# Optimization experiments

Hardware: AMD Instinct MI355X
Metric: run time of the kernel (lower is better)

The kernel has to match this reference:

```python
import jax, jax.numpy as jnp
import numpy as np


def setup_inputs() -> dict:
    key = jax.random.key(0)
    k1, k2 = jax.random.split(key)
    x = jax.random.normal(k1, (128, 128, 256), dtype=jnp.float32)
    embed = jax.random.normal(k2, (16384, 256), dtype=jnp.float32)
    return {"x": x, "embed": embed}


BETA = 0.25


def reference(x, embed):
    dim = embed.shape[1]
    n_embed = embed.shape[0]
    latent = x.reshape(-1, dim)  # [N, d]
    # squared euclidean distance: ||z||^2 - 2 z.e^T + ||e||^2  -> [N, K]
    dist = (
        jnp.sum(latent * latent, axis=1, keepdims=True)
        - 2.0 * jnp.einsum("nd,kd->nk", latent, embed)
        + jnp.sum(embed * embed, axis=1)[None, :]
    )
    embed_ind = jnp.argmax(-dist, axis=1)  # [N]
    # one-hot histogram of code usage (segment_sum == onehot.sum(0))
    embed_onehot_sum = jax.ops.segment_sum(
        jnp.ones_like(embed_ind, dtype=jnp.int32), embed_ind, num_segments=n_embed
    )
    unused_codes = jnp.sum(embed_onehot_sum == 0)
    x_q = embed[embed_ind].reshape(x.shape)
    quant_loss = jnp.mean((x_q - jax.lax.stop_gradient(x)) ** 2) + BETA * jnp.mean(
        (x - jax.lax.stop_gradient(x_q)) ** 2
    )
    # straight-through estimator
    x_q = x + jax.lax.stop_gradient(x_q - x)
    embed_ind = embed_ind.reshape(x.shape[:-1])
    return (x_q, quant_loss, unused_codes, embed_ind)
```

## Files before the change

kernel.cpp:

```cpp
#include <hip/hip_runtime.h>

#define N_LAT 16384
#define N_EMB 16384
#define DIM   256
#define XQ_ELEMS (N_LAT * DIM)

typedef __attribute__((ext_vector_type(8))) _Float16 f16x8;
typedef __attribute__((ext_vector_type(4))) float    f32x4;

#define SWZ(a) ((a) ^ ((((a) >> 6) & 7) << 4))

#define GLD16(g, l) __builtin_amdgcn_global_load_lds( \
    (const __attribute__((address_space(1))) unsigned int*)(g), \
    (__attribute__((address_space(3))) unsigned int*)(l), 16, 0, 0)


__global__ __launch_bounds__(256) void k_convert(const float* __restrict__ src,
                                                 char* __restrict__ hi,
                                                 char* __restrict__ lo,
                                                 float* __restrict__ norm) {
    const int gid = blockIdx.x * 256 + threadIdx.x;
    const int row = gid >> 5, k8 = gid & 31;
    const float* s = src + (size_t)row * DIM + k8 * 8;
    float f[8];
    *reinterpret_cast<float4*>(&f[0]) = *reinterpret_cast<const float4*>(s);
    *reinterpret_cast<float4*>(&f[4]) = *reinterpret_cast<const float4*>(s + 4);
    f16x8 hv, lv;
    double nrm = 0.0;
#pragma unroll
    for (int m = 0; m < 8; ++m) {
        const _Float16 h = (_Float16)f[m];
        hv[m] = h;
        lv[m] = (_Float16)(f[m] - (float)h);
        nrm += (double)f[m] * (double)f[m];
    }
    const int dst = ((row >> 7) * 8 + (k8 >> 2)) * 8192 + SWZ((row & 127) * 64 + (k8 & 3) * 16);
    *reinterpret_cast<f16x8*>(hi + dst) = hv;
    *reinterpret_cast<f16x8*>(lo + dst) = lv;
    if (norm) {
#pragma unroll
        for (int m = 16; m; m >>= 1) nrm += __shfl_xor(nrm, m, 64);
        if (k8 == 0) norm[row] = (float)nrm;
    }
}

__global__ __launch_bounds__(256) void k_argmin(const char* __restrict__ xhi,
                                                const char* __restrict__ xlo,
                                                const char* __restrict__ ehi,
                                                const char* __restrict__ elo,
                                                const float* __restrict__ enorm,
                                                unsigned long long* __restrict__ best) {
    __shared__ char smem[65536];
    char* const sm = smem;

    const int tid = threadIdx.x;
    const int w   = tid >> 6;
    const int l   = tid & 63;
    const int lg  = l >> 4;
    const int lr  = l & 15;

    const int row0 = blockIdx.x * 128;
    const int kc   = blockIdx.y;

    const size_t lane16 = (size_t)(w * 2048 + l * 16);
    const size_t gA  = (size_t)blockIdx.x * 65536 + lane16;
    const size_t gB0 = (size_t)kc * 8 * 65536 + lane16;

    auto STAGE = [&](int ct_, int ks_, int half) {
        const int    o  = half * 32768 + w * 2048;
        const size_t ga = gA + (size_t)ks_ * 8192;
        const size_t gb = gB0 + (size_t)ct_ * 65536 + (size_t)ks_ * 8192;
#pragma unroll
        for (int q = 0; q < 2; ++q) {
            GLD16(xhi + ga + q * 1024, sm + o +         q * 1024);
            GLD16(xlo + ga + q * 1024, sm + o +  8192 + q * 1024);
            GLD16(ehi + gb + q * 1024, sm + o + 16384 + q * 1024);
            GLD16(elo + gb + q * 1024, sm + o + 24576 + q * 1024);
        }
    };

    int aoff[2];
#pragma unroll
    for (int i = 0; i < 2; ++i)
        aoff[i] = SWZ((w * 32 + i * 16 + lr) * 64 + lg * 16);
    int boff[8];
#pragma unroll
    for (int j = 0; j < 8; ++j)
        boff[j] = SWZ((j * 16 + lr) * 64 + lg * 16);

    unsigned long long pmin[2][4];
#pragma unroll
    for (int i = 0; i < 2; ++i)
#pragma unroll
        for (int t = 0; t < 4; ++t) pmin[i][t] = ~0ULL;

    STAGE(0, 0, 0);
    __syncthreads();
    int half = 0;

    for (int ct = 0; ct < 8; ++ct) {
        f32x4 acc[2][8];
#pragma unroll
        for (int i = 0; i < 2; ++i)
#pragma unroll
            for (int j = 0; j < 8; ++j) acc[i][j] = (f32x4)0.0f;

        for (int ks = 0; ks < 8; ++ks) {
            int nks = ks + 1, nct = ct;
            if (nks == 8) { nks = 0; ++nct; }
            if (nct < 8) STAGE(nct, nks, half ^ 1);

            const int hb = half * 32768;
            f16x8 ah[2], al[2];
#pragma unroll
            for (int i = 0; i < 2; ++i) {
                ah[i] = *reinterpret_cast<const f16x8*>(sm + hb +        aoff[i]);
                al[i] = *reinterpret_cast<const f16x8*>(sm + hb + 8192 + aoff[i]);
            }
#pragma unroll
            for (int j = 0; j < 8; ++j) {
                const f16x8 bh = *reinterpret_cast<const f16x8*>(sm + hb + 16384 + boff[j]);
                const f16x8 bl = *reinterpret_cast<const f16x8*>(sm + hb + 24576 + boff[j]);
#pragma unroll
                for (int i = 0; i < 2; ++i) {
                    acc[i][j] = __builtin_amdgcn_mfma_f32_16x16x32_f16(ah[i], bh, acc[i][j], 0, 0, 0);
                    acc[i][j] = __builtin_amdgcn_mfma_f32_16x16x32_f16(ah[i], bl, acc[i][j], 0, 0, 0);
                    acc[i][j] = __builtin_amdgcn_mfma_f32_16x16x32_f16(al[i], bh, acc[i][j], 0, 0, 0);
                }
            }
            __syncthreads();
            half ^= 1;
        }
        const int colbase = kc * 1024 + ct * 128;
#pragma unroll
        for (int j = 0; j < 8; ++j) {
            const int   col = colbase + j * 16 + lr;
            const float s   = enorm[col];
#pragma unroll
            for (int i = 0; i < 2; ++i)
#pragma unroll
                for (int t = 0; t < 4; ++t) {
                    const float v = fmaf(-2.0f, acc[i][j][t], s);
                    unsigned u = __float_as_uint(v);
                    u = (u & 0x80000000u) ? ~u : (u | 0x80000000u);
                    const unsigned long long p = ((unsigned long long)u << 32) | (unsigned)col;
                    if (p < pmin[i][t]) pmin[i][t] = p;
                }
        }
    }
#pragma unroll
    for (int i = 0; i < 2; ++i)
#pragma unroll
        for (int t = 0; t < 4; ++t) {
            unsigned long long p = pmin[i][t];
#pragma unroll
            for (int m = 1; m < 16; m <<= 1) {
                const unsigned long long q = __shfl_xor(p, m, 64);
                if (q < p) p = q;
            }
            if (lr == 0) {
                const int row = row0 + w * 32 + i * 16 + lg * 4 + t;
                atomicMin(&best[row], p);
            }
        }
}

__global__ __launch_bounds__(256) void k_gather(const float* __restrict__ x,
                                                const float* __restrict__ embed,
                                                const unsigned long long* __restrict__ best,
                                                float* __restrict__ out,
                                                int* __restrict__ hist,
                                                double* __restrict__ bsum) {
    __shared__ double partial[4];
    const int row = blockIdx.x;
    const int t   = threadIdx.x;
    const int idx = (int)(best[row] & 0xFFFFFFFFULL);
    const float e  = embed[(size_t)idx * DIM + t];
    const float xv = x[(size_t)row * DIM + t];
    const float d  = e - xv;
    out[(size_t)row * DIM + t] = xv + d;
    double sq = (double)d * (double)d;
#pragma unroll
    for (int m = 32; m; m >>= 1) sq += __shfl_xor(sq, m, 64);
    const int lane = t & 63, wv = t >> 6;
    if (lane == 0) partial[wv] = sq;
    __syncthreads();
    if (t == 0) {
        bsum[row] = partial[0] + partial[1] + partial[2] + partial[3];
        atomicAdd(&hist[idx], 1);
        out[XQ_ELEMS + 2 + row] = (float)idx;
    }
}

__global__ __launch_bounds__(256) void k_final(const int* __restrict__ hist,
                                               const double* __restrict__ bsum,
                                               float* __restrict__ out) {
    __shared__ int    cpart[4];
    __shared__ double spart[4];
    const int t = threadIdx.x;
    int cnt = 0; double s = 0.0;
    for (int i = t; i < N_EMB; i += 256) {
        cnt += (hist[i] == 0) ? 1 : 0;
        s += bsum[i];
    }
#pragma unroll
    for (int m = 32; m; m >>= 1) {
        cnt += __shfl_xor(cnt, m, 64);
        s   += __shfl_xor(s, m, 64);
    }
    const int lane = t & 63, wv = t >> 6;
    if (lane == 0) { cpart[wv] = cnt; spart[wv] = s; }
    __syncthreads();
    if (t == 0) {
        const double sse = spart[0] + spart[1] + spart[2] + spart[3];
        out[XQ_ELEMS + 0] = (float)(1.25 * sse / (double)XQ_ELEMS);
        out[XQ_ELEMS + 1] = (float)(cpart[0] + cpart[1] + cpart[2] + cpart[3]);
    }
}

extern "C" void kernel_launch(void* const* d_in, const int* in_sizes, int n_in,
                              void* d_out, int out_size, void* d_ws, size_t ws_size,
                              hipStream_t stream) {
    const float* x     = (const float*)d_in[0];
    const float* embed = (const float*)d_in[1];
    float* out = (float*)d_out;

    char* ws = (char*)d_ws;
    float*              enorm = (float*)(ws + 0);
    unsigned long long* best  = (unsigned long long*)(ws + 65536);
    int*                hist  = (int*)(ws + 196608);
    double*             bsum  = (double*)(ws + 262144);
    char*               xhi   = ws + 393216;
    char*               xlo   = xhi + 8388608;
    char*               ehi   = xlo + 8388608;
    char*               elo   = ehi + 8388608;

    hipMemsetAsync(best, 0xFF, N_LAT * sizeof(unsigned long long), stream);
    hipMemsetAsync(hist, 0x00, N_EMB * sizeof(int), stream);

    k_convert<<<2048, 256, 0, stream>>>(x, xhi, xlo, nullptr);
    k_convert<<<2048, 256, 0, stream>>>(embed, ehi, elo, enorm);
    k_argmin <<<dim3(128, 16), 256, 0, stream>>>(xhi, xlo, ehi, elo, enorm, best);
    k_gather <<<N_LAT, 256, 0, stream>>>(x, embed, best, out, hist, bsum);
    k_final  <<<1, 256, 0, stream>>>(hist, bsum, out);
}
```

Baseline: 563.2 us.

## Load latent A fragments directly from global into registers, halve LDS staging

```diff
diff --git a/kernel.cpp b/kernel.cpp
--- a/kernel.cpp
+++ b/kernel.cpp
@@ -13,6 +13,8 @@
 #define GLD16(g, l) __builtin_amdgcn_global_load_lds( \
     (const __attribute__((address_space(1))) unsigned int*)(g), \
     (__attribute__((address_space(3))) unsigned int*)(l), 16, 0, 0)
+
+#define MFMA16(a, b, c) __builtin_amdgcn_mfma_f32_16x16x32_f16((a), (b), (c), 0, 0, 0)
 
 
 __global__ __launch_bounds__(256) void k_convert(const float* __restrict__ src,
@@ -50,7 +52,7 @@
                                                 const char* __restrict__ elo,
                                                 const float* __restrict__ enorm,
                                                 unsigned long long* __restrict__ best) {
-    __shared__ char smem[65536];
+    __shared__ char smem[32768];
     char* const sm = smem;
 
     const int tid = threadIdx.x;
@@ -63,19 +65,15 @@
     const int kc   = blockIdx.y;
 
     const size_t lane16 = (size_t)(w * 2048 + l * 16);
-    const size_t gA  = (size_t)blockIdx.x * 65536 + lane16;
-    const size_t gB0 = (size_t)kc * 8 * 65536 + lane16;
-
-    auto STAGE = [&](int ct_, int ks_, int half) {
-        const int    o  = half * 32768 + w * 2048;
-        const size_t ga = gA + (size_t)ks_ * 8192;
+    const size_t gB0    = (size_t)kc * 8 * 65536 + lane16;
+
+    auto STAGE = [&](int ct_, int ks_, int half_) {
+        const int    o  = half_ * 16384 + w * 2048;
         const size_t gb = gB0 + (size_t)ct_ * 65536 + (size_t)ks_ * 8192;
 #pragma unroll
         for (int q = 0; q < 2; ++q) {
-            GLD16(xhi + ga + q * 1024, sm + o +         q * 1024);
-            GLD16(xlo + ga + q * 1024, sm + o +  8192 + q * 1024);
-            GLD16(ehi + gb + q * 1024, sm + o + 16384 + q * 1024);
-            GLD16(elo + gb + q * 1024, sm + o + 24576 + q * 1024);
+            GLD16(ehi + gb + q * 1024, sm + o +        q * 1024);
+            GLD16(elo + gb + q * 1024, sm + o + 8192 + q * 1024);
         }
     };
 
@@ -88,12 +86,25 @@
     for (int j = 0; j < 8; ++j)
         boff[j] = SWZ((j * 16 + lr) * 64 + lg * 16);
 
+    const size_t abase = (size_t)blockIdx.x * 65536;
+    auto LOADA = [&](int ks_, f16x8& h0, f16x8& h1, f16x8& l0, f16x8& l1) {
+        const size_t b = abase + (size_t)ks_ * 8192;
+        h0 = *reinterpret_cast<const f16x8*>(xhi + b + aoff[0]);
+        h1 = *reinterpret_cast<const f16x8*>(xhi + b + aoff[1]);
+        l0 = *reinterpret_cast<const f16x8*>(xlo + b + aoff[0]);
+        l1 = *reinterpret_cast<const f16x8*>(xlo + b + aoff[1]);
+    };
+
     unsigned long long pmin[2][4];
 #pragma unroll
     for (int i = 0; i < 2; ++i)
 #pragma unroll
         for (int t = 0; t < 4; ++t) pmin[i][t] = ~0ULL;
 
+    f16x8 cah0, cah1, cal0, cal1;
+    f16x8 nah0, nah1, nal0, nal1;
+
+    LOADA(0, cah0, cah1, cal0, cal1);
     STAGE(0, 0, 0);
     __syncthreads();
     int half = 0;
@@ -105,31 +116,30 @@
 #pragma unroll
             for (int j = 0; j < 8; ++j) acc[i][j] = (f32x4)0.0f;
 
+#pragma unroll
         for (int ks = 0; ks < 8; ++ks) {
             int nks = ks + 1, nct = ct;
             if (nks == 8) { nks = 0; ++nct; }
-            if (nct < 8) STAGE(nct, nks, half ^ 1);
-
-            const int hb = half * 32768;
-            f16x8 ah[2], al[2];
-#pragma unroll
-            for (int i = 0; i < 2; ++i) {
-                ah[i] = *reinterpret_cast<const f16x8*>(sm + hb +        aoff[i]);
-                al[i] = *reinterpret_cast<const f16x8*>(sm + hb + 8192 + aoff[i]);
-            }
+            const bool more = (nct < 8);
+            if (more) {
+                LOADA(nks, nah0, nah1, nal0, nal1);
+                STAGE(nct, nks, half ^ 1);
+            }
+            const int hb = half * 16384;
 #pragma unroll
             for (int j = 0; j < 8; ++j) {
-                const f16x8 bh = *reinterpret_cast<const f16x8*>(sm + hb + 16384 + boff[j]);
-                const f16x8 bl = *reinterpret_cast<const f16x8*>(sm + hb + 24576 + boff[j]);
-#pragma unroll
-                for (int i = 0; i < 2; ++i) {
-                    acc[i][j] = __builtin_amdgcn_mfma_f32_16x16x32_f16(ah[i], bh, acc[i][j], 0, 0, 0);
-                    acc[i][j] = __builtin_amdgcn_mfma_f32_16x16x32_f16(ah[i], bl, acc[i][j], 0, 0, 0);
-                    acc[i][j] = __builtin_amdgcn_mfma_f32_16x16x32_f16(al[i], bh, acc[i][j], 0, 0, 0);
-                }
+                const f16x8 bh = *reinterpret_cast<const f16x8*>(sm + hb +        boff[j]);
+                const f16x8 bl = *reinterpret_cast<const f16x8*>(sm + hb + 8192 + boff[j]);
+                acc[0][j] = MFMA16(cah0, bh, acc[0][j]);
+                acc[0][j] = MFMA16(cah0, bl, acc[0][j]);
+                acc[0][j] = MFMA16(cal0, bh, acc[0][j]);
+                acc[1][j] = MFMA16(cah1, bh, acc[1][j]);
+                acc[1][j] = MFMA16(cah1, bl, acc[1][j]);
+                acc[1][j] = MFMA16(cal1, bh, acc[1][j]);
             }
             __syncthreads();
             half ^= 1;
+            if (more) { cah0 = nah0; cah1 = nah1; cal0 = nal0; cal1 = nal1; }
         }
         const int colbase = kc * 1024 + ct * 128;
 #pragma unroll
```

Result: slower. 604.1 us (+7.3%).
